# Performance work log

Measured on AMD Instinct MI355X. Metric: run time of the kernel, lower is better.

The kernel has to match this reference:

```python
import jax, jax.numpy as jnp
import numpy as np

N, E, G = 20000, 320000, 16
IN, HID, OUT, HEADS = 256, 64, 256, 4
D0 = HID * HEADS  # 256, output dim of layer 0 (concat)


def _p(key, shape, scale=0.05):
    return (jax.random.normal(key, shape, dtype=jnp.float32) * scale)


def setup_inputs() -> dict:
    key = jax.random.key(0)
    ks = jax.random.split(key, 24)
    x = jax.random.normal(ks[0], (N, IN), dtype=jnp.float32)
    edge_index = jax.random.randint(ks[1], (2, E), 0, N, dtype=jnp.int64)
    batch = jnp.sort(jax.random.randint(ks[2], (N,), 0, G, dtype=jnp.int64))
    d = {"x": x, "edge_index": edge_index, "batch": batch}
    # Layer 0: TransformerConv(256 -> 64, heads=4, concat=True, beta=True)
    d["Wq0"] = _p(ks[3], (IN, D0)); d["bq0"] = jnp.zeros((D0,), jnp.float32)
    d["Wk0"] = _p(ks[4], (IN, D0)); d["bk0"] = jnp.zeros((D0,), jnp.float32)
    d["Wv0"] = _p(ks[5], (IN, D0)); d["bv0"] = jnp.zeros((D0,), jnp.float32)
    d["Ws0"] = _p(ks[6], (IN, D0)); d["bs0"] = jnp.zeros((D0,), jnp.float32)
    d["Wb0"] = _p(ks[7], (3 * D0, 1))
    d["g0"] = jnp.ones((D0,), jnp.float32); d["b0"] = jnp.zeros((D0,), jnp.float32)
    # Layer 1: TransformerConv(256 -> 256, heads=1, concat=False, beta=True)
    d["Wq1"] = _p(ks[8], (D0, OUT)); d["bq1"] = jnp.zeros((OUT,), jnp.float32)
    d["Wk1"] = _p(ks[9], (D0, OUT)); d["bk1"] = jnp.zeros((OUT,), jnp.float32)
    d["Wv1"] = _p(ks[10], (D0, OUT)); d["bv1"] = jnp.zeros((OUT,), jnp.float32)
    d["Ws1"] = _p(ks[11], (D0, OUT)); d["bs1"] = jnp.zeros((OUT,), jnp.float32)
    d["Wb1"] = _p(ks[12], (3 * OUT, 1))
    d["g1"] = jnp.ones((OUT,), jnp.float32); d["b1"] = jnp.zeros((OUT,), jnp.float32)
    return d


def _transformer_conv(x, src, dst, Wq, bq, Wk, bk, Wv, bv, Ws, bs, Wb, H, C, concat):
    n = x.shape[0]
    q = (x @ Wq + bq).reshape(n, H, C)
    k = (x @ Wk + bk).reshape(n, H, C)
    v = (x @ Wv + bv).reshape(n, H, C)
    # per-edge attention logits [E, H]
    alpha = (q[dst] * k[src]).sum(-1) / jnp.sqrt(jnp.asarray(C, jnp.float32))
    # segment softmax over incoming edges of each dst node
    m = jax.ops.segment_max(alpha, dst, num_segments=n)  # [N, H]
    a = jnp.exp(alpha - m[dst])
    s = jax.ops.segment_sum(a, dst, num_segments=n)  # [N, H]
    a = a / s[dst]
    out = jax.ops.segment_sum(a[:, :, None] * v[src], dst, num_segments=n)  # [N,H,C]
    out = out.reshape(n, H * C) if concat else out.mean(axis=1)
    # beta-gated skip connection
    r = x @ Ws + bs
    g = jax.nn.sigmoid(jnp.concatenate([out, r, out - r], axis=-1) @ Wb)  # [N,1]
    return g * r + (1.0 - g) * out


def _layer_norm(x, g, b, eps=1e-5):
    mu = x.mean(-1, keepdims=True)
    var = x.var(-1, keepdims=True)
    return (x - mu) * jax.lax.rsqrt(var + eps) * g + b


def reference(x, edge_index, batch,
              Wq0, bq0, Wk0, bk0, Wv0, bv0, Ws0, bs0, Wb0, g0, b0,
              Wq1, bq1, Wk1, bk1, Wv1, bv1, Ws1, bs1, Wb1, g1, b1):
    src, dst = edge_index[0], edge_index[1]
    h = _transformer_conv(x, src, dst, Wq0, bq0, Wk0, bk0, Wv0, bv0, Ws0, bs0, Wb0, HEADS, HID, True)
    h = jax.nn.relu(_layer_norm(h, g0, b0))  # dropout is identity at inference
    h = _transformer_conv(h, src, dst, Wq1, bq1, Wk1, bk1, Wv1, bv1, Ws1, bs1, Wb1, 1, OUT, False)
    h = _layer_norm(h, g1, b1)
    # global mean pool over graphs
    sums = jax.ops.segment_sum(h, batch, num_segments=G)
    counts = jax.ops.segment_sum(jnp.ones((h.shape[0],), h.dtype), batch, num_segments=G)
    return sums / jnp.maximum(counts, 1.0)[:, None]
```

## Files before the change

### kernel.cpp

```cpp
#include <hip/hip_runtime.h>
#include <hip/hip_bf16.h>


#define DEVFN static __device__ __forceinline__

typedef __attribute__((ext_vector_type(4))) float f32x4;
typedef __attribute__((ext_vector_type(2))) float f32x2;
typedef __attribute__((ext_vector_type(8))) short bf16x8;

DEVFN float bfu2f(unsigned short u) {
    union { unsigned int i; float f; } t; t.i = ((unsigned)u) << 16; return t.f;
}
DEVFN float4 ldb4(const __hip_bfloat16* p) {
    ushort4 u = *reinterpret_cast<const ushort4*>(p);
    return make_float4(bfu2f(u.x), bfu2f(u.y), bfu2f(u.z), bfu2f(u.w));
}
DEVFN unsigned short f2bu(float f) {
    __hip_bfloat16 b = __float2bfloat16(f);
    return __builtin_bit_cast(unsigned short, b);
}
DEVFN void stb4(__hip_bfloat16* p, float4 v) {
    ushort4 u;
    u.x = f2bu(v.x); u.y = f2bu(v.y); u.z = f2bu(v.z); u.w = f2bu(v.w);
    *reinterpret_cast<ushort4*>(p) = u;
}
DEVFN float4 f8x4_to_f4(unsigned u) {
    const f32x2 lo = __builtin_amdgcn_cvt_pk_f32_fp8((int)u, false);
    const f32x2 hi = __builtin_amdgcn_cvt_pk_f32_fp8((int)u, true);
    return make_float4(lo.x, lo.y, hi.x, hi.y);
}

__global__ __launch_bounds__(256)
void f2b_kernel(const float* __restrict__ in, __hip_bfloat16* __restrict__ out, int n4)
{
    const int i = blockIdx.x * 256 + threadIdx.x;
    if (i >= n4) return;
    const float4 v = *reinterpret_cast<const float4*>(in + (size_t)i * 4);
    stb4(out + (size_t)i * 4, v);
}

__global__ __launch_bounds__(256)
void wconv_kernel(const float* __restrict__ W0, const float* __restrict__ W1,
                  const float* __restrict__ W2, const float* __restrict__ W3,
                  const float* __restrict__ W4, const float* __restrict__ W5,
                  const float* __restrict__ W6, const float* __restrict__ W7,
                  __hip_bfloat16* __restrict__ Wt)
{
    const float* W;
    switch (blockIdx.y) {
        case 0: W = W0; break; case 1: W = W1; break;
        case 2: W = W2; break; case 3: W = W3; break;
        case 4: W = W4; break; case 5: W = W5; break;
        case 6: W = W6; break; default: W = W7; break;
    }
    const int k = blockIdx.x;
    const int c = threadIdx.x;
    Wt[(size_t)blockIdx.y * 65536 + (size_t)c * 256 + k] =
        __float2bfloat16(W[(size_t)k * 256 + c]);
}

#define SWZ(r, kb) ((r) * 256 + ((kb) ^ (((r) & 7) << 4)))
#define TSTRIDE 272

__global__ __launch_bounds__(256)
void gemm_mfma_kernel(const __hip_bfloat16* __restrict__ A, int M,
                      const __hip_bfloat16* __restrict__ Wt,
                      const float* __restrict__ b0, const float* __restrict__ b1,
                      const float* __restrict__ b2, const float* __restrict__ b3,
                      void* __restrict__ O0, void* __restrict__ O1,
                      void* __restrict__ O2, void* __restrict__ O3,
                      int s0, int s1, int s2, int s3,
                      int f0, int f1, int f2, int f3)
{
    const int q8   = gridDim.x >> 3;
    const int wgid = (blockIdx.x & 7) * q8 + (blockIdx.x >> 3);
    const int rowblk = wgid >> 3;
    const int rem    = wgid & 7;
    const int colblk = rem >> 2;
    const int z      = rem & 3;

    const float* bias; void* O; int rs, isf8;
    switch (z) {
        case 0:  bias = b0; O = O0; rs = s0; isf8 = f0; break;
        case 1:  bias = b1; O = O1; rs = s1; isf8 = f1; break;
        case 2:  bias = b2; O = O2; rs = s2; isf8 = f2; break;
        default: bias = b3; O = O3; rs = s3; isf8 = f3; break;
    }
    const __hip_bfloat16* Wz = Wt + (size_t)z * 65536;

    __shared__ char Sh[2 * 128 * 256];
    char* As = Sh;
    char* Bs = Sh + 128 * 256;

    const int tid  = threadIdx.x;
    const int row0 = rowblk * 128;
    const int col0 = colblk * 128;
    const int wid  = tid >> 6, lane = tid & 63;
    const int wr   = wid >> 1, wc = wid & 1;
    const int lrow = lane & 15, kg = lane >> 4;

    const int chunk = tid & 15;
    const int rsub  = tid >> 4;

    f32x4 acc[4][4] = {};

    for (int k0 = 0; k0 < 256; k0 += 128) {
        #pragma unroll
        for (int p = 0; p < 8; ++p) {
            const int r  = p * 16 + rsub;
            const int gr = row0 + r;
            ulonglong2 av = {0ull, 0ull};
            if (gr < M)
                av = *reinterpret_cast<const ulonglong2*>(A + (size_t)gr * 256 + k0 + chunk * 8);
            *reinterpret_cast<ulonglong2*>(As + SWZ(r, chunk * 16)) = av;

            const ulonglong2 bv = *reinterpret_cast<const ulonglong2*>(
                Wz + (size_t)(col0 + r) * 256 + k0 + chunk * 8);
            *reinterpret_cast<ulonglong2*>(Bs + SWZ(r, chunk * 16)) = bv;
        }
        __syncthreads();

        #pragma unroll
        for (int kk = 0; kk < 128; kk += 32) {
            const int kbyte = kk * 2 + kg * 16;
            bf16x8 af[4], bfr[4];
            #pragma unroll
            for (int m = 0; m < 4; ++m) {
                const int r = wr * 64 + m * 16 + lrow;
                af[m] = *reinterpret_cast<const bf16x8*>(As + SWZ(r, kbyte));
            }
            #pragma unroll
            for (int n = 0; n < 4; ++n) {
                const int c = wc * 64 + n * 16 + lrow;
                bfr[n] = *reinterpret_cast<const bf16x8*>(Bs + SWZ(c, kbyte));
            }
            #pragma unroll
            for (int m = 0; m < 4; ++m)
                #pragma unroll
                for (int n = 0; n < 4; ++n)
                    acc[m][n] = __builtin_amdgcn_mfma_f32_16x16x32_bf16(
                        af[m], bfr[n], acc[m][n], 0, 0, 0);
        }
        __syncthreads();
    }

    #pragma unroll
    for (int m = 0; m < 4; ++m) {
        #pragma unroll
        for (int j = 0; j < 4; ++j) {
            const int rr = wr * 64 + m * 16 + kg * 4 + j;
            #pragma unroll
            for (int n = 0; n < 4; ++n) {
                const int cc = wc * 64 + n * 16 + lrow;
                const float v = acc[m][n][j] + bias[col0 + cc];
                *reinterpret_cast<unsigned short*>(Sh + rr * TSTRIDE + cc * 2) = f2bu(v);
            }
        }
    }
    __syncthreads();

    const int row  = tid >> 1;
    const int half = tid & 1;
    const int grow = row0 + row;
    if (grow >= M) return;
    const char* src = Sh + row * TSTRIDE + half * 128;

    if (isf8) {
        unsigned char* dst = (unsigned char*)O + (size_t)grow * rs + col0 + half * 64;
        #pragma unroll
        for (int i2 = 0; i2 < 4; ++i2) {
            uint4 w;
            unsigned tmp[4];
            #pragma unroll
            for (int c8 = 0; c8 < 2; ++c8) {
                const bf16x8 e = *reinterpret_cast<const bf16x8*>(src + (i2 * 2 + c8) * 16);
                const int p0 = __builtin_amdgcn_cvt_pk_fp8_f32(
                    bfu2f((unsigned short)e[0]), bfu2f((unsigned short)e[1]), 0, false);
                const int p1 = __builtin_amdgcn_cvt_pk_fp8_f32(
                    bfu2f((unsigned short)e[2]), bfu2f((unsigned short)e[3]), 0, false);
                const int p2 = __builtin_amdgcn_cvt_pk_fp8_f32(
                    bfu2f((unsigned short)e[4]), bfu2f((unsigned short)e[5]), 0, false);
                const int p3 = __builtin_amdgcn_cvt_pk_fp8_f32(
                    bfu2f((unsigned short)e[6]), bfu2f((unsigned short)e[7]), 0, false);
                tmp[c8 * 2 + 0] = (unsigned)(p0 & 0xFFFF) | ((unsigned)(p1 & 0xFFFF) << 16);
                tmp[c8 * 2 + 1] = (unsigned)(p2 & 0xFFFF) | ((unsigned)(p3 & 0xFFFF) << 16);
            }
            w.x = tmp[0]; w.y = tmp[1]; w.z = tmp[2]; w.w = tmp[3];
            *reinterpret_cast<uint4*>(dst + i2 * 16) = w;
        }
    } else {
        char* dst = (char*)((__hip_bfloat16*)O + (size_t)grow * rs + col0 + half * 64);
        #pragma unroll
        for (int i = 0; i < 8; ++i)
            *reinterpret_cast<ulonglong2*>(dst + i * 16) =
                *reinterpret_cast<const ulonglong2*>(src + i * 16);
    }
}

__global__ __launch_bounds__(256)
void hist_kernel(const int* __restrict__ ei, int E, int* __restrict__ deg)
{
    const int e = blockIdx.x * 256 + threadIdx.x;
    if (e < E) atomicAdd(&deg[ei[E + e]], 1);
}

__global__ __launch_bounds__(256)
void gcount_kernel(const int* __restrict__ batch, int N, int* __restrict__ gcount)
{
    __shared__ int h[16];
    if (threadIdx.x < 16) h[threadIdx.x] = 0;
    __syncthreads();
    const int n = blockIdx.x * 256 + threadIdx.x;
    if (n < N) atomicAdd(&h[batch[n]], 1);
    __syncthreads();
    if (threadIdx.x < 16 && h[threadIdx.x] != 0)
        atomicAdd(&gcount[threadIdx.x], h[threadIdx.x]);
}

__global__ __launch_bounds__(64)
void gstart_kernel(const int* __restrict__ gcount, int* __restrict__ gstart)
{
    if (threadIdx.x == 0) {
        int o = 0;
        for (int g = 0; g < 16; ++g) { gstart[g] = o; o += gcount[g]; }
        gstart[16] = o;
    }
}

__global__ __launch_bounds__(1024)
void scan_kernel(const int* __restrict__ deg, int* __restrict__ row_start, int n)
{
    __shared__ int wsum[16];
    __shared__ int wincl[16];
    const int tid  = threadIdx.x;
    const int w    = tid >> 6;
    const int lane = tid & 63;
    if (tid == 0) row_start[0] = 0;
    int offset = 0;
    for (int base = 0; base < n; base += 1024) {
        const int idx = base + tid;
        int s = (idx < n) ? deg[idx] : 0;
        #pragma unroll
        for (int d = 1; d < 64; d <<= 1) {
            const int t = __shfl_up(s, d, 64);
            if (lane >= d) s += t;
        }
        if (lane == 63) wsum[w] = s;
        __syncthreads();
        if (tid < 16) {
            int si = wsum[tid];
            #pragma unroll
            for (int d = 1; d < 16; d <<= 1) {
                const int u = __shfl_up(si, d, 64);
                if (tid >= d) si += u;
            }
            wincl[tid] = si;
        }
        __syncthreads();
        const int woff = (w > 0) ? wincl[w - 1] : 0;
        if (idx < n) row_start[idx + 1] = offset + woff + s;
        offset += wincl[15];
        __syncthreads();
    }
}

__global__ __launch_bounds__(256)
void fill_kernel(const int* __restrict__ ei, int E,
                 const int* __restrict__ row_start,
                 int* __restrict__ cursor, int* __restrict__ csr_src)
{
    const int e = blockIdx.x * 256 + threadIdx.x;
    if (e >= E) return;
    const int s = ei[e];
    const int d = ei[E + e];
    const int pos = atomicAdd(&cursor[d], 1);
    csr_src[row_start[d] + pos] = s;
}

template <int HL, bool RELU, bool OUTB>
__global__ __launch_bounds__(512)
void attn_kernel(const __hip_bfloat16* __restrict__ Q,
                 const unsigned char* __restrict__ KV,
                 const __hip_bfloat16* __restrict__ R,
                 const float* __restrict__ Wb, const float* __restrict__ lng,
                 const float* __restrict__ lnb,
                 const int* __restrict__ row_start, const int* __restrict__ csr_src,
                 __hip_bfloat16* __restrict__ outb, float* __restrict__ outf,
                 int N, float scale)
{
    __shared__ float4 sAcc[4][64];
    __shared__ float  sSum[4][64];

    const int w    = threadIdx.x >> 6;
    const int lane = threadIdx.x & 63;
    const int slot = w >> 1;
    const int half = w & 1;
    const int node = blockIdx.x * 4 + slot;
    const bool active = node < N;

    const int d4 = lane * 4;
    float4 q4 = make_float4(0.f, 0.f, 0.f, 0.f);
    int beg = 0, end = 0;
    if (active) {
        q4  = ldb4(Q + (size_t)node * 256 + d4);
        beg = row_start[node];
        end = row_start[node + 1];
    }

    float4 acc0 = make_float4(0.f, 0.f, 0.f, 0.f);
    float4 acc1 = make_float4(0.f, 0.f, 0.f, 0.f);
    float  ssum0 = 0.f, ssum1 = 0.f;

    int i = beg + half;
    for (; i + 2 < end; i += 4) {
        const int sa = csr_src[i];
        const int sb = csr_src[i + 2];
        const unsigned* pa = reinterpret_cast<const unsigned*>(KV + (size_t)sa * 512 + d4);
        const unsigned* pb = reinterpret_cast<const unsigned*>(KV + (size_t)sb * 512 + d4);
        const unsigned kua = pa[0];
        const unsigned vua = pa[64];
        const unsigned kub = pb[0];
        const unsigned vub = pb[64];
        const float4 ka = f8x4_to_f4(kua);
        const float4 va = f8x4_to_f4(vua);
        const float4 kb = f8x4_to_f4(kub);
        const float4 vb = f8x4_to_f4(vub);
        float pa_ = q4.x * ka.x + q4.y * ka.y + q4.z * ka.z + q4.w * ka.w;
        float pb_ = q4.x * kb.x + q4.y * kb.y + q4.z * kb.z + q4.w * kb.w;
        #pragma unroll
        for (int m = 1; m < HL; m <<= 1) {
            pa_ += __shfl_xor(pa_, m, 64);
            pb_ += __shfl_xor(pb_, m, 64);
        }
        const float aa = __expf(pa_ * scale);
        const float ab = __expf(pb_ * scale);
        ssum0 += aa; ssum1 += ab;
        acc0.x = fmaf(aa, va.x, acc0.x); acc0.y = fmaf(aa, va.y, acc0.y);
        acc0.z = fmaf(aa, va.z, acc0.z); acc0.w = fmaf(aa, va.w, acc0.w);
        acc1.x = fmaf(ab, vb.x, acc1.x); acc1.y = fmaf(ab, vb.y, acc1.y);
        acc1.z = fmaf(ab, vb.z, acc1.z); acc1.w = fmaf(ab, vb.w, acc1.w);
    }
    if (i < end) {
        const int sa = csr_src[i];
        const unsigned* pa = reinterpret_cast<const unsigned*>(KV + (size_t)sa * 512 + d4);
        const unsigned kua = pa[0];
        const unsigned vua = pa[64];
        const float4 ka = f8x4_to_f4(kua);
        const float4 va = f8x4_to_f4(vua);
        float pa_ = q4.x * ka.x + q4.y * ka.y + q4.z * ka.z + q4.w * ka.w;
        #pragma unroll
        for (int m = 1; m < HL; m <<= 1) pa_ += __shfl_xor(pa_, m, 64);
        const float aa = __expf(pa_ * scale);
        ssum0 += aa;
        acc0.x = fmaf(aa, va.x, acc0.x); acc0.y = fmaf(aa, va.y, acc0.y);
        acc0.z = fmaf(aa, va.z, acc0.z); acc0.w = fmaf(aa, va.w, acc0.w);
    }

    float4 acc = make_float4(acc0.x + acc1.x, acc0.y + acc1.y,
                             acc0.z + acc1.z, acc0.w + acc1.w);
    float ssum = ssum0 + ssum1;

    if (half == 1) {
        sAcc[slot][lane] = acc;
        sSum[slot][lane] = ssum;
    }
    __syncthreads();
    if (half == 1 || !active) return;

    const float4 oa = sAcc[slot][lane];
    acc.x += oa.x; acc.y += oa.y; acc.z += oa.z; acc.w += oa.w;
    ssum += sSum[slot][lane];

    float4 o4 = make_float4(0.f, 0.f, 0.f, 0.f);
    if (ssum > 0.f) {
        const float is = 1.f / ssum;
        o4.x = acc.x * is; o4.y = acc.y * is; o4.z = acc.z * is; o4.w = acc.w * is;
    }

    const float4 r4  = ldb4(R + (size_t)node * 256 + d4);
    const float4 wb0 = *reinterpret_cast<const float4*>(Wb + d4);
    const float4 wb1 = *reinterpret_cast<const float4*>(Wb + 256 + d4);
    const float4 wb2 = *reinterpret_cast<const float4*>(Wb + 512 + d4);
    float z = o4.x * wb0.x + o4.y * wb0.y + o4.z * wb0.z + o4.w * wb0.w
            + r4.x * wb1.x + r4.y * wb1.y + r4.z * wb1.z + r4.w * wb1.w
            + (o4.x - r4.x) * wb2.x + (o4.y - r4.y) * wb2.y
            + (o4.z - r4.z) * wb2.z + (o4.w - r4.w) * wb2.w;
    #pragma unroll
    for (int m = 1; m < 64; m <<= 1) z += __shfl_xor(z, m, 64);
    const float g = 1.f / (1.f + __expf(-z));

    float4 h4;
    h4.x = g * r4.x + (1.f - g) * o4.x;
    h4.y = g * r4.y + (1.f - g) * o4.y;
    h4.z = g * r4.z + (1.f - g) * o4.z;
    h4.w = g * r4.w + (1.f - g) * o4.w;

    float s1 = h4.x + h4.y + h4.z + h4.w;
    float s2 = h4.x * h4.x + h4.y * h4.y + h4.z * h4.z + h4.w * h4.w;
    #pragma unroll
    for (int m = 1; m < 64; m <<= 1) {
        s1 += __shfl_xor(s1, m, 64);
        s2 += __shfl_xor(s2, m, 64);
    }
    const float mu  = s1 * (1.f / 256.f);
    const float var = s2 * (1.f / 256.f) - mu * mu;
    const float inv = rsqrtf(var + 1e-5f);

    const float4 ga = *reinterpret_cast<const float4*>(lng + d4);
    const float4 be = *reinterpret_cast<const float4*>(lnb + d4);
    h4.x = (h4.x - mu) * inv * ga.x + be.x;
    h4.y = (h4.y - mu) * inv * ga.y + be.y;
    h4.z = (h4.z - mu) * inv * ga.z + be.z;
    h4.w = (h4.w - mu) * inv * ga.w + be.w;

    if (RELU) {
        h4.x = fmaxf(h4.x, 0.f);
        h4.y = fmaxf(h4.y, 0.f);
        h4.z = fmaxf(h4.z, 0.f);
        h4.w = fmaxf(h4.w, 0.f);
    }

    if (OUTB) stb4(outb + (size_t)node * 256 + d4, h4);
    else      *reinterpret_cast<float4*>(outf + (size_t)node * 256 + d4) = h4;
}

__global__ __launch_bounds__(256)
void pool_partial_kernel(const float* __restrict__ h, const int* __restrict__ gstart,
                         float* __restrict__ partial)
{
    const int s    = blockIdx.x;
    const int g    = blockIdx.y;
    const int tid  = threadIdx.x;
    const int quad = tid & 63;
    const int sub  = tid >> 6;

    const int beg = gstart[g];
    const int cnt = gstart[g + 1] - beg;

    f32x4 acc = {0.f, 0.f, 0.f, 0.f};
    for (int i = s * 4 + sub; i < cnt; i += 64) {
        const f32x4 v = *reinterpret_cast<const f32x4*>(
            h + (size_t)(beg + i) * 256 + quad * 4);
        acc += v;
    }

    __shared__ f32x4 sh[4][64];
    sh[sub][quad] = acc;
    __syncthreads();
    if (sub == 0) {
        const f32x4 r = sh[0][quad] + sh[1][quad] + sh[2][quad] + sh[3][quad];
        *reinterpret_cast<f32x4*>(partial + ((size_t)(g * 16 + s) * 64 + quad) * 4) = r;
    }
}

__global__ __launch_bounds__(256)
void pool_final_kernel(const float* __restrict__ partial, const int* __restrict__ gcount,
                       float* __restrict__ out)
{
    const int g = blockIdx.x;
    const int d = threadIdx.x;
    float sum = 0.f;
    #pragma unroll
    for (int s = 0; s < 16; ++s)
        sum += partial[(size_t)(g * 16 + s) * 256 + d];
    out[(size_t)g * 256 + d] = sum / (float)max(gcount[g], 1);
}

extern "C" void kernel_launch(void* const* d_in, const int* in_sizes, int n_in,
                              void* d_out, int out_size, void* d_ws, size_t ws_size,
                              hipStream_t stream)
{
    const float* x     = (const float*)d_in[0];
    const int*   ei    = (const int*)d_in[1];
    const int*   batch = (const int*)d_in[2];
    const float* Wq0 = (const float*)d_in[3];  const float* bq0 = (const float*)d_in[4];
    const float* Wk0 = (const float*)d_in[5];  const float* bk0 = (const float*)d_in[6];
    const float* Wv0 = (const float*)d_in[7];  const float* bv0 = (const float*)d_in[8];
    const float* Ws0 = (const float*)d_in[9];  const float* bs0 = (const float*)d_in[10];
    const float* Wb0 = (const float*)d_in[11];
    const float* g0  = (const float*)d_in[12]; const float* b0  = (const float*)d_in[13];
    const float* Wq1 = (const float*)d_in[14]; const float* bq1 = (const float*)d_in[15];
    const float* Wk1 = (const float*)d_in[16]; const float* bk1 = (const float*)d_in[17];
    const float* Wv1 = (const float*)d_in[18]; const float* bv1 = (const float*)d_in[19];
    const float* Ws1 = (const float*)d_in[20]; const float* bs1 = (const float*)d_in[21];
    const float* Wb1 = (const float*)d_in[22];
    const float* g1  = (const float*)d_in[23]; const float* b1  = (const float*)d_in[24];

    const int N = in_sizes[0] / 256;
    const int E = in_sizes[1] / 2;
    const int G = 16;
    const size_t NM = (size_t)N * 256;

    __hip_bfloat16* bws = (__hip_bfloat16*)d_ws;
    __hip_bfloat16* xb  = bws;
    __hip_bfloat16* qb  = xb  + NM;
    __hip_bfloat16* rb  = qb  + NM;
    __hip_bfloat16* h0b = rb  + NM;
    __hip_bfloat16* wt  = h0b + NM;
    unsigned char* kvb  = (unsigned char*)(wt + 8 * 65536);
    float* h1f     = (float*)(kvb + (size_t)N * 512);
    float* partial = h1f + NM;
    int* deg       = (int*)(partial + 16 * 16 * 256);
    int* row_start = deg + N;
    int* cursor    = row_start + N + 1;
    int* gcount    = cursor + N;
    int* gstart    = gcount + G;
    int* csr_src   = gstart + 17;

    const size_t zbytes = ((size_t)N + (N + 1) + N + G + 17) * sizeof(int);
    hipMemsetAsync(deg, 0, zbytes, stream);

    const int eb = (E + 255) / 256;
    const int nb = (N + 255) / 256;

    f2b_kernel<<<(int)((NM / 4 + 255) / 256), 256, 0, stream>>>(x, xb, (int)(NM / 4));
    wconv_kernel<<<dim3(256, 8), 256, 0, stream>>>(Wq0, Wk0, Wv0, Ws0,
                                                   Wq1, Wk1, Wv1, Ws1, wt);

    hist_kernel<<<eb, 256, 0, stream>>>(ei, E, deg);
    gcount_kernel<<<nb, 256, 0, stream>>>(batch, N, gcount);
    gstart_kernel<<<1, 64, 0, stream>>>(gcount, gstart);
    scan_kernel<<<1, 1024, 0, stream>>>(deg, row_start, N);
    fill_kernel<<<eb, 256, 0, stream>>>(ei, E, row_start, cursor, csr_src);

    const int nrb   = (N + 127) / 128;
    const int ggrid = nrb * 8;
    const int agrid = (N + 3) / 4;

    gemm_mfma_kernel<<<ggrid, 256, 0, stream>>>(xb, N, wt,
        bq0, bk0, bv0, bs0,
        qb, kvb, kvb + 256, rb,
        256, 512, 512, 256,
        0, 1, 1, 0);
    attn_kernel<16, true, true><<<agrid, 512, 0, stream>>>(
        qb, kvb, rb, Wb0, g0, b0, row_start, csr_src, h0b, nullptr, N, 0.125f);

    gemm_mfma_kernel<<<ggrid, 256, 0, stream>>>(h0b, N, wt + 4 * 65536,
        bq1, bk1, bv1, bs1,
        qb, kvb, kvb + 256, rb,
        256, 512, 512, 256,
        0, 1, 1, 0);
    attn_kernel<64, false, false><<<agrid, 512, 0, stream>>>(
        qb, kvb, rb, Wb1, g1, b1, row_start, csr_src, nullptr, h1f, N, 0.0625f);

    pool_partial_kernel<<<dim3(16, 16), 256, 0, stream>>>(h1f, gstart, partial);
    pool_final_kernel<<<16, 256, 0, stream>>>(partial, gcount, (float*)d_out);
}
```

Before: 237.5 us.

## Split each wave into four edge groups with 16-byte-per-lane KV loads

The attention kernel now uses one wave per destination node instead of two waves per node. The wave is split into four groups of 16 lanes, and each group handles a different edge. Each lane loads 16 fp8 K and V values with uint4 loads instead of 4 bytes, which cuts the shuffle depth of the dot-product reduction and removes the LDS exchange and __syncthreads between half-waves. It costs more registers (16-float accumulators and q), a cross-group shuffle reduction at the end, and an epilogue where only a quarter of the lanes are active.

```diff
diff --git a/kernel.cpp b/kernel.cpp
--- a/kernel.cpp
+++ b/kernel.cpp
@@ -28,6 +28,37 @@
     const f32x2 lo = __builtin_amdgcn_cvt_pk_f32_fp8((int)u, false);
     const f32x2 hi = __builtin_amdgcn_cvt_pk_f32_fp8((int)u, true);
     return make_float4(lo.x, lo.y, hi.x, hi.y);
+}
+
+DEVFN float dot16(const float* q, uint4 u) {
+    const float4 f0 = f8x4_to_f4(u.x);
+    const float4 f1 = f8x4_to_f4(u.y);
+    const float4 f2 = f8x4_to_f4(u.z);
+    const float4 f3 = f8x4_to_f4(u.w);
+    float p;
+    p = q[0] * f0.x;            p = fmaf(q[1],  f0.y, p);
+    p = fmaf(q[2],  f0.z, p);   p = fmaf(q[3],  f0.w, p);
+    p = fmaf(q[4],  f1.x, p);   p = fmaf(q[5],  f1.y, p);
+    p = fmaf(q[6],  f1.z, p);   p = fmaf(q[7],  f1.w, p);
+    p = fmaf(q[8],  f2.x, p);   p = fmaf(q[9],  f2.y, p);
+    p = fmaf(q[10], f2.z, p);   p = fmaf(q[11], f2.w, p);
+    p = fmaf(q[12], f3.x, p);   p = fmaf(q[13], f3.y, p);
+    p = fmaf(q[14], f3.z, p);   p = fmaf(q[15], f3.w, p);
+    return p;
+}
+DEVFN void accum16(float* acc, uint4 u, float a) {
+    const float4 f0 = f8x4_to_f4(u.x);
+    const float4 f1 = f8x4_to_f4(u.y);
+    const float4 f2 = f8x4_to_f4(u.z);
+    const float4 f3 = f8x4_to_f4(u.w);
+    acc[0]  = fmaf(a, f0.x, acc[0]);  acc[1]  = fmaf(a, f0.y, acc[1]);
+    acc[2]  = fmaf(a, f0.z, acc[2]);  acc[3]  = fmaf(a, f0.w, acc[3]);
+    acc[4]  = fmaf(a, f1.x, acc[4]);  acc[5]  = fmaf(a, f1.y, acc[5]);
+    acc[6]  = fmaf(a, f1.z, acc[6]);  acc[7]  = fmaf(a, f1.w, acc[7]);
+    acc[8]  = fmaf(a, f2.x, acc[8]);  acc[9]  = fmaf(a, f2.y, acc[9]);
+    acc[10] = fmaf(a, f2.z, acc[10]); acc[11] = fmaf(a, f2.w, acc[11]);
+    acc[12] = fmaf(a, f3.x, acc[12]); acc[13] = fmaf(a, f3.y, acc[13]);
+    acc[14] = fmaf(a, f3.z, acc[14]); acc[15] = fmaf(a, f3.w, acc[15]);
 }
 
 __global__ __launch_bounds__(256)
@@ -277,8 +308,8 @@
     csr_src[row_start[d] + pos] = s;
 }
 
-template <int HL, bool RELU, bool OUTB>
-__global__ __launch_bounds__(512)
+template <int NSH, bool RELU, bool OUTB>
+__global__ __launch_bounds__(256)
 void attn_kernel(const __hip_bfloat16* __restrict__ Q,
                  const unsigned char* __restrict__ KV,
                  const __hip_bfloat16* __restrict__ R,
@@ -288,117 +319,109 @@
                  __hip_bfloat16* __restrict__ outb, float* __restrict__ outf,
                  int N, float scale)
 {
-    __shared__ float4 sAcc[4][64];
-    __shared__ float  sSum[4][64];
-
-    const int w    = threadIdx.x >> 6;
+    const int wv   = threadIdx.x >> 6;
     const int lane = threadIdx.x & 63;
-    const int slot = w >> 1;
-    const int half = w & 1;
-    const int node = blockIdx.x * 4 + slot;
-    const bool active = node < N;
-
-    const int d4 = lane * 4;
-    float4 q4 = make_float4(0.f, 0.f, 0.f, 0.f);
-    int beg = 0, end = 0;
-    if (active) {
-        q4  = ldb4(Q + (size_t)node * 256 + d4);
-        beg = row_start[node];
-        end = row_start[node + 1];
-    }
-
-    float4 acc0 = make_float4(0.f, 0.f, 0.f, 0.f);
-    float4 acc1 = make_float4(0.f, 0.f, 0.f, 0.f);
-    float  ssum0 = 0.f, ssum1 = 0.f;
-
-    int i = beg + half;
-    for (; i + 2 < end; i += 4) {
+    const int g    = lane >> 4;
+    const int s    = lane & 15;
+    const int node = blockIdx.x * 4 + wv;
+    if (node >= N) return;
+
+    float q[16];
+    {
+        const bf16x8 a = *reinterpret_cast<const bf16x8*>(Q + (size_t)node * 256 + s * 16);
+        const bf16x8 b = *reinterpret_cast<const bf16x8*>(Q + (size_t)node * 256 + s * 16 + 8);
+        #pragma unroll
+        for (int j = 0; j < 8; ++j) {
+            q[j]     = bfu2f((unsigned short)a[j]);
+            q[8 + j] = bfu2f((unsigned short)b[j]);
+        }
+    }
+
+    const int beg = row_start[node];
+    const int end = row_start[node + 1];
+
+    float acc[16] = {};
+    float ssum = 0.f;
+
+    int i = beg + g;
+    for (; i + 4 < end; i += 8) {
         const int sa = csr_src[i];
-        const int sb = csr_src[i + 2];
-        const unsigned* pa = reinterpret_cast<const unsigned*>(KV + (size_t)sa * 512 + d4);
-        const unsigned* pb = reinterpret_cast<const unsigned*>(KV + (size_t)sb * 512 + d4);
-        const unsigned kua = pa[0];
-        const unsigned vua = pa[64];
-        const unsigned kub = pb[0];
-        const unsigned vub = pb[64];
-        const float4 ka = f8x4_to_f4(kua);
-        const float4 va = f8x4_to_f4(vua);
-        const float4 kb = f8x4_to_f4(kub);
-        const float4 vb = f8x4_to_f4(vub);
-        float pa_ = q4.x * ka.x + q4.y * ka.y + q4.z * ka.z + q4.w * ka.w;
-        float pb_ = q4.x * kb.x + q4.y * kb.y + q4.z * kb.z + q4.w * kb.w;
-        #pragma unroll
-        for (int m = 1; m < HL; m <<= 1) {
-            pa_ += __shfl_xor(pa_, m, 64);
-            pb_ += __shfl_xor(pb_, m, 64);
-        }
-        const float aa = __expf(pa_ * scale);
-        const float ab = __expf(pb_ * scale);
-        ssum0 += aa; ssum1 += ab;
-        acc0.x = fmaf(aa, va.x, acc0.x); acc0.y = fmaf(aa, va.y, acc0.y);
-        acc0.z = fmaf(aa, va.z, acc0.z); acc0.w = fmaf(aa, va.w, acc0.w);
-        acc1.x = fmaf(ab, vb.x, acc1.x); acc1.y = fmaf(ab, vb.y, acc1.y);
-        acc1.z = fmaf(ab, vb.z, acc1.z); acc1.w = fmaf(ab, vb.w, acc1.w);
+        const int sb = csr_src[i + 4];
+        const uint4 ka = *reinterpret_cast<const uint4*>(KV + (size_t)sa * 512 + s * 16);
+        const uint4 va = *reinterpret_cast<const uint4*>(KV + (size_t)sa * 512 + 256 + s * 16);
+        const uint4 kb = *reinterpret_cast<const uint4*>(KV + (size_t)sb * 512 + s * 16);
+        const uint4 vb = *reinterpret_cast<const uint4*>(KV + (size_t)sb * 512 + 256 + s * 16);
+        float pa = dot16(q, ka);
+        float pb = dot16(q, kb);
+        #pragma unroll
+        for (int m = 1; m < (1 << NSH); m <<= 1) {
+            pa += __shfl_xor(pa, m, 64);
+            pb += __shfl_xor(pb, m, 64);
+        }
+        const float aa = __expf(pa * scale);
+        const float ab = __expf(pb * scale);
+        ssum += aa + ab;
+        accum16(acc, va, aa);
+        accum16(acc, vb, ab);
     }
     if (i < end) {
         const int sa = csr_src[i];
-        const unsigned* pa = reinterpret_cast<const unsigned*>(KV + (size_t)sa * 512 + d4);
-        const unsigned kua = pa[0];
-        const unsigned vua = pa[64];
-        const float4 ka = f8x4_to_f4(kua);
-        const float4 va = f8x4_to_f4(vua);
-        float pa_ = q4.x * ka.x + q4.y * ka.y + q4.z * ka.z + q4.w * ka.w;
-        #pragma unroll
-        for (int m = 1; m < HL; m <<= 1) pa_ += __shfl_xor(pa_, m, 64);
-        const float aa = __expf(pa_ * scale);
-        ssum0 += aa;
-        acc0.x = fmaf(aa, va.x, acc0.x); acc0.y = fmaf(aa, va.y, acc0.y);
-        acc0.z = fmaf(aa, va.z, acc0.z); acc0.w = fmaf(aa, va.w, acc0.w);
-    }
-
-    float4 acc = make_float4(acc0.x + acc1.x, acc0.y + acc1.y,
-                             acc0.z + acc1.z, acc0.w + acc1.w);
-    float ssum = ssum0 + ssum1;
-
-    if (half == 1) {
-        sAcc[slot][lane] = acc;
-        sSum[slot][lane] = ssum;
-    }
-    __syncthreads();
-    if (half == 1 || !active) return;
-
-    const float4 oa = sAcc[slot][lane];
-    acc.x += oa.x; acc.y += oa.y; acc.z += oa.z; acc.w += oa.w;
-    ssum += sSum[slot][lane];
-
-    float4 o4 = make_float4(0.f, 0.f, 0.f, 0.f);
-    if (ssum > 0.f) {
-        const float is = 1.f / ssum;
-        o4.x = acc.x * is; o4.y = acc.y * is; o4.z = acc.z * is; o4.w = acc.w * is;
-    }
-
-    const float4 r4  = ldb4(R + (size_t)node * 256 + d4);
-    const float4 wb0 = *reinterpret_cast<const float4*>(Wb + d4);
-    const float4 wb1 = *reinterpret_cast<const float4*>(Wb + 256 + d4);
-    const float4 wb2 = *reinterpret_cast<const float4*>(Wb + 512 + d4);
-    float z = o4.x * wb0.x + o4.y * wb0.y + o4.z * wb0.z + o4.w * wb0.w
-            + r4.x * wb1.x + r4.y * wb1.y + r4.z * wb1.z + r4.w * wb1.w
-            + (o4.x - r4.x) * wb2.x + (o4.y - r4.y) * wb2.y
-            + (o4.z - r4.z) * wb2.z + (o4.w - r4.w) * wb2.w;
-    #pragma unroll
-    for (int m = 1; m < 64; m <<= 1) z += __shfl_xor(z, m, 64);
-    const float g = 1.f / (1.f + __expf(-z));
-
-    float4 h4;
-    h4.x = g * r4.x + (1.f - g) * o4.x;
-    h4.y = g * r4.y + (1.f - g) * o4.y;
-    h4.z = g * r4.z + (1.f - g) * o4.z;
-    h4.w = g * r4.w + (1.f - g) * o4.w;
-
-    float s1 = h4.x + h4.y + h4.z + h4.w;
-    float s2 = h4.x * h4.x + h4.y * h4.y + h4.z * h4.z + h4.w * h4.w;
-    #pragma unroll
-    for (int m = 1; m < 64; m <<= 1) {
+        const uint4 ka = *reinterpret_cast<const uint4*>(KV + (size_t)sa * 512 + s * 16);
+        const uint4 va = *reinterpret_cast<const uint4*>(KV + (size_t)sa * 512 + 256 + s * 16);
+        float pa = dot16(q, ka);
+        #pragma unroll
+        for (int m = 1; m < (1 << NSH); m <<= 1) pa += __shfl_xor(pa, m, 64);
+        const float aa = __expf(pa * scale);
+        ssum += aa;
+        accum16(acc, va, aa);
+    }
+
+    ssum += __shfl_xor(ssum, 16, 64);
+    ssum += __shfl_xor(ssum, 32, 64);
+    #pragma unroll
+    for (int j = 0; j < 16; ++j) {
+        acc[j] += __shfl_xor(acc[j], 16, 64);
+        acc[j] += __shfl_xor(acc[j], 32, 64);
+    }
+
+    if (g != 0) return;
+
+    const float is = (ssum > 0.f) ? 1.f / ssum : 0.f;
+    float o[16];
+    #pragma unroll
+    for (int j = 0; j < 16; ++j) o[j] = acc[j] * is;
+
+    float r[16];
+    {
+        const bf16x8 a = *reinterpret_cast<const bf16x8*>(R + (size_t)node * 256 + s * 16);
+        const bf16x8 b = *reinterpret_cast<const bf16x8*>(R + (size_t)node * 256 + s * 16 + 8);
+        #pragma unroll
+        for (int j = 0; j < 8; ++j) {
+            r[j]     = bfu2f((unsigned short)a[j]);
+            r[8 + j] = bfu2f((unsigned short)b[j]);
+        }
+    }
+
+    float z = 0.f;
+    #pragma unroll
+    for (int j = 0; j < 16; ++j) {
+        const int d = s * 16 + j;
+        z += o[j] * Wb[d] + r[j] * Wb[256 + d] + (o[j] - r[j]) * Wb[512 + d];
+    }
+    #pragma unroll
+    for (int m = 1; m < 16; m <<= 1) z += __shfl_xor(z, m, 64);
+    const float gg = 1.f / (1.f + __expf(-z));
+
+    float h[16];
+    float s1 = 0.f, s2 = 0.f;
+    #pragma unroll
+    for (int j = 0; j < 16; ++j) {
+        h[j] = gg * r[j] + (1.f - gg) * o[j];
+        s1 += h[j];
+        s2 += h[j] * h[j];
+    }
+    #pragma unroll
+    for (int m = 1; m < 16; m <<= 1) {
         s1 += __shfl_xor(s1, m, 64);
         s2 += __shfl_xor(s2, m, 64);
     }
@@ -406,22 +429,26 @@
     const float var = s2 * (1.f / 256.f) - mu * mu;
     const float inv = rsqrtf(var + 1e-5f);
 
-    const float4 ga = *reinterpret_cast<const float4*>(lng + d4);
-    const float4 be = *reinterpret_cast<const float4*>(lnb + d4);
-    h4.x = (h4.x - mu) * inv * ga.x + be.x;
-    h4.y = (h4.y - mu) * inv * ga.y + be.y;
-    h4.z = (h4.z - mu) * inv * ga.z + be.z;
-    h4.w = (h4.w - mu) * inv * ga.w + be.w;
-
-    if (RELU) {
-        h4.x = fmaxf(h4.x, 0.f);
-        h4.y = fmaxf(h4.y, 0.f);
-        h4.z = fmaxf(h4.z, 0.f);
-        h4.w = fmaxf(h4.w, 0.f);
-    }
-
-    if (OUTB) stb4(outb + (size_t)node * 256 + d4, h4);
-    else      *reinterpret_cast<float4*>(outf + (size_t)node * 256 + d4) = h4;
+    #pragma unroll
+    for (int j = 0; j < 16; ++j) {
+        const int d = s * 16 + j;
+        h[j] = (h[j] - mu) * inv * lng[d] + lnb[d];
+        if (RELU) h[j] = fmaxf(h[j], 0.f);
+    }
+
+    if (OUTB) {
+        __hip_bfloat16* dst = outb + (size_t)node * 256 + s * 16;
+        stb4(dst,      make_float4(h[0],  h[1],  h[2],  h[3]));
+        stb4(dst + 4,  make_float4(h[4],  h[5],  h[6],  h[7]));
+        stb4(dst + 8,  make_float4(h[8],  h[9],  h[10], h[11]));
+        stb4(dst + 12, make_float4(h[12], h[13], h[14], h[15]));
+    } else {
+        float* dst = outf + (size_t)node * 256 + s * 16;
+        #pragma unroll
+        for (int c4 = 0; c4 < 4; ++c4)
+            *reinterpret_cast<float4*>(dst + c4 * 4) =
+                make_float4(h[c4 * 4], h[c4 * 4 + 1], h[c4 * 4 + 2], h[c4 * 4 + 3]);
+    }
 }
 
 __global__ __launch_bounds__(256)
@@ -532,7 +559,7 @@
         qb, kvb, kvb + 256, rb,
         256, 512, 512, 256,
         0, 1, 1, 0);
-    attn_kernel<16, true, true><<<agrid, 512, 0, stream>>>(
+    attn_kernel<2, true, true><<<agrid, 256, 0, stream>>>(
         qb, kvb, rb, Wb0, g0, b0, row_start, csr_src, h0b, nullptr, N, 0.125f);
 
     gemm_mfma_kernel<<<ggrid, 256, 0, stream>>>(h0b, N, wt + 4 * 65536,
@@ -540,7 +567,7 @@
         qb, kvb, kvb + 256, rb,
         256, 512, 512, 256,
         0, 1, 1, 0);
-    attn_kernel<64, false, false><<<agrid, 512, 0, stream>>>(
+    attn_kernel<4, false, false><<<agrid, 256, 0, stream>>>(
         qb, kvb, rb, Wb1, g1, b1, row_start, csr_src, nullptr, h1f, N, 0.0625f);
 
     pool_partial_kernel<<<dim3(16, 16), 256, 0, stream>>>(h1f, gstart, partial);
```

New measurement: 235.3 us. No clear change (-0.9%).
